# Optimization experiments

Measured on AMD Instinct MI355X. Metric: run time of the kernel, lower is better.

The kernel has to match this reference:

```python
import jax, jax.numpy as jnp
import numpy as np

B, S, D, H = 2, 2048, 1024, 16
DH = D // H  # depth per head = 64


def setup_inputs() -> dict:
    key = jax.random.key(0)
    ks = jax.random.split(key, 5)
    sc = 0.02
    return {
        "x": jax.random.normal(ks[0], (B, S, D), dtype=jnp.float32),
        "Wq": jax.random.normal(ks[1], (D, D), dtype=jnp.float32) * sc,
        "bq": jnp.zeros((D,), dtype=jnp.float32),
        "Wk": jax.random.normal(ks[2], (D, D), dtype=jnp.float32) * sc,
        "bk": jnp.zeros((D,), dtype=jnp.float32),
        "Wv": jax.random.normal(ks[3], (D, D), dtype=jnp.float32) * sc,
        "bv": jnp.zeros((D,), dtype=jnp.float32),
        "Wo": jax.random.normal(ks[4], (D, D), dtype=jnp.float32) * sc,
        "bo": jnp.zeros((D,), dtype=jnp.float32),
    }


def _split_heads(t):
    # [B,S,D] -> [B,H,S,DH]
    return t.reshape(B, S, H, DH).transpose(0, 2, 1, 3)


def reference(x, Wq, bq, Wk, bk, Wv, bv, Wo, bo):
    q = _split_heads(x @ Wq + bq)
    k = _split_heads(x @ Wk + bk)
    v = _split_heads(x @ Wv + bv)
    scale = 1.0 / jnp.sqrt(jnp.float32(DH))
    logits = jnp.einsum("bhqd,bhkd->bhqk", q, k) * scale  # [B,H,S,S]
    attn = jax.nn.softmax(logits, axis=-1)
    ctx = jnp.einsum("bhqk,bhkd->bhqd", attn, v)
    ctx = ctx.transpose(0, 2, 1, 3).reshape(B, S, D)
    # dropout is identity at inference
    return ctx @ Wo + bo
```

## Files before the change

### kernel.cpp

```cpp
#include <hip/hip_runtime.h>
#include <hip/hip_bf16.h>

#define S_LEN   2048
#define D_MODEL 1024
#define NHEAD   16
#define DHEAD   64
#define M_ROWS  4096
#define BHEADS  32
#define MEG     1048576

typedef __attribute__((ext_vector_type(8)))  short short8;
typedef __attribute__((ext_vector_type(4)))  float f32x4;
typedef __attribute__((ext_vector_type(16))) float f32x16;
typedef __attribute__((ext_vector_type(4)))  unsigned short us4;
typedef __attribute__((ext_vector_type(2)))  unsigned int uint2v;
typedef __attribute__((ext_vector_type(4)))  unsigned int uint4v;

extern "C" __device__ float __ocml_native_exp2_f32(float);

__device__ __forceinline__ unsigned short f2b(float f) {
    unsigned int u = __builtin_bit_cast(unsigned int, f);
    return (unsigned short)((u + 0x7FFFu + ((u >> 16) & 1u)) >> 16);
}

__device__ __forceinline__ unsigned int cvtpk(float lo, float hi) {
    unsigned int r;
    asm("v_cvt_pk_bf16_f32 %0, %1, %2" : "=v"(r) : "v"(lo), "v"(hi));
    return r;
}

__device__ __forceinline__ float b2f(unsigned short b) {
    return __builtin_bit_cast(float, (unsigned int)b << 16);
}

#define GLOAD16(gp, lp) __builtin_amdgcn_global_load_lds(                     \
        (const __attribute__((address_space(1))) void*)(gp),                  \
        (__attribute__((address_space(3))) void*)(lp), 16, 0, 0)

#define STAGE_OFS(lane) ((((lane) & 3) ^ (((lane) >> 3) & 3)) * 8)

#define ZERO16(v) do { _Pragma("unroll")                                      \
    for (int z_ = 0; z_ < 16; ++z_) (v)[z_] = 0.f; } while (0)

__global__ __launch_bounds__(256) void prep(
    const float* __restrict__ x, unsigned short* __restrict__ xb,
    const float* __restrict__ Wq, const float* __restrict__ Wk,
    const float* __restrict__ Wv, const float* __restrict__ Wo,
    unsigned short* __restrict__ Wqt, unsigned short* __restrict__ Wkt,
    unsigned short* __restrict__ Wvt, unsigned short* __restrict__ Wot)
{
    const int z = blockIdx.z;
    const int tx = threadIdx.x, ty = threadIdx.y;
    if (z == 4) {
        const int blk = blockIdx.y * 32 + blockIdx.x;
        const int base = (blk * 256 + ty * 32 + tx) * 4;
        #pragma unroll
        for (int r = 0; r < 4; ++r) {
            const int i = base + r * (M_ROWS * D_MODEL / 4);
            const float4 v = *(const float4*)&x[i];
            us4 o;
            o.x = f2b(v.x); o.y = f2b(v.y); o.z = f2b(v.z); o.w = f2b(v.w);
            *(us4*)&xb[i] = o;
        }
        return;
    }
    __shared__ float tile[32][33];
    const float* W = z == 0 ? Wq : (z == 1 ? Wk : (z == 2 ? Wv : Wo));
    unsigned short* Wt = z == 0 ? Wqt : (z == 1 ? Wkt : (z == 2 ? Wvt : Wot));
    const int n0 = blockIdx.x * 32, k0 = blockIdx.y * 32;
    #pragma unroll
    for (int i = 0; i < 4; ++i)
        tile[ty + i * 8][tx] = W[(size_t)(k0 + ty + i * 8) * D_MODEL + n0 + tx];
    __syncthreads();
    #pragma unroll
    for (int i = 0; i < 4; ++i)
        Wt[(size_t)(n0 + ty + i * 8) * D_MODEL + k0 + tx] = f2b(tile[tx][ty + i * 8]);
}

__global__ __launch_bounds__(256) void gemm_qkv(
    const unsigned short* __restrict__ xb,
    const unsigned short* __restrict__ Wqt, const unsigned short* __restrict__ Wkt,
    const unsigned short* __restrict__ Wvt,
    const float* __restrict__ bq, const float* __restrict__ bk,
    const float* __restrict__ bv,
    unsigned short* __restrict__ Qb, unsigned short* __restrict__ Kb,
    unsigned short* __restrict__ Vt)
{
    __shared__ unsigned short As[2][128][32];
    __shared__ unsigned short Bs[2][128][32];

    const int z = blockIdx.z;
    const unsigned short* Wt = z == 0 ? Wqt : (z == 1 ? Wkt : Wvt);
    const float* bias = z == 0 ? bq : (z == 1 ? bk : bv);

    const int t = threadIdx.x, lane = t & 63, w = t >> 6;
    const int wm = w >> 1, wn = w & 1;
    const int bm = blockIdx.y * 128, bn = blockIdx.x * 128;
    const int lr = lane >> 2, lc = STAGE_OFS(lane);
    const int lm = lane & 15, quad = lane >> 4;
    const int qo = (quad ^ ((lm >> 1) & 3)) * 8;

    f32x4 acc[4][4] = {};

    #pragma unroll
    for (int i = 0; i < 2; ++i) {
        const int c = 2 * w + i;
        GLOAD16(xb + (size_t)(bm + c * 16 + lr) * D_MODEL + lc, &As[0][c * 16][0]);
        GLOAD16(Wt + (size_t)(bn + c * 16 + lr) * D_MODEL + lc, &Bs[0][c * 16][0]);
    }
    __syncthreads();

    for (int it = 0; it < 32; ++it) {
        const int cur = it & 1;
        if (it + 1 < 32) {
            const int kt = (it + 1) * 32;
            #pragma unroll
            for (int i = 0; i < 2; ++i) {
                const int c = 2 * w + i;
                GLOAD16(xb + (size_t)(bm + c * 16 + lr) * D_MODEL + kt + lc,
                        &As[cur ^ 1][c * 16][0]);
                GLOAD16(Wt + (size_t)(bn + c * 16 + lr) * D_MODEL + kt + lc,
                        &Bs[cur ^ 1][c * 16][0]);
            }
        }

        short8 af[4], bfr[4];
        #pragma unroll
        for (int mi = 0; mi < 4; ++mi)
            af[mi] = *(const short8*)&As[cur][wm * 64 + mi * 16 + lm][qo];
        #pragma unroll
        for (int ni = 0; ni < 4; ++ni)
            bfr[ni] = *(const short8*)&Bs[cur][wn * 64 + ni * 16 + lm][qo];
        #pragma unroll
        for (int mi = 0; mi < 4; ++mi)
            #pragma unroll
            for (int ni = 0; ni < 4; ++ni)
                acc[mi][ni] = __builtin_amdgcn_mfma_f32_16x16x32_bf16(
                    af[mi], bfr[ni], acc[mi][ni], 0, 0, 0);

        __syncthreads();
    }

    float bb[4];
    #pragma unroll
    for (int ni = 0; ni < 4; ++ni)
        bb[ni] = bias[bn + wn * 64 + ni * 16 + lm];
    const float scale = (z == 0) ? 0.18033688011112042f : 1.0f;

    if (z < 2) {
        unsigned short* Out = (z == 0) ? Qb : Kb;
        #pragma unroll
        for (int mi = 0; mi < 4; ++mi)
            #pragma unroll
            for (int r = 0; r < 4; ++r) {
                const int row = bm + wm * 64 + mi * 16 + quad * 4 + r;
                const int b = row >> 11, s = row & 2047;
                #pragma unroll
                for (int ni = 0; ni < 4; ++ni) {
                    const int col = bn + wn * 64 + ni * 16 + lm;
                    const int h = col >> 6, d = col & 63;
                    Out[(((size_t)(b * NHEAD + h)) * S_LEN + s) * DHEAD + d] =
                        f2b((acc[mi][ni][r] + bb[ni]) * scale);
                }
            }
    } else {
        #pragma unroll
        for (int mi = 0; mi < 4; ++mi) {
            const int row0 = bm + wm * 64 + mi * 16 + quad * 4;
            const int b = row0 >> 11, s0 = row0 & 2047;
            #pragma unroll
            for (int ni = 0; ni < 4; ++ni) {
                const int col = bn + wn * 64 + ni * 16 + lm;
                const int h = col >> 6, d = col & 63;
                us4 pk;
                pk.x = f2b(acc[mi][ni][0] + bb[ni]);
                pk.y = f2b(acc[mi][ni][1] + bb[ni]);
                pk.z = f2b(acc[mi][ni][2] + bb[ni]);
                pk.w = f2b(acc[mi][ni][3] + bb[ni]);
                *(us4*)&Vt[(((size_t)(b * NHEAD + h)) * DHEAD + d) * S_LEN + s0] = pk;
            }
        }
    }
}

__global__ __launch_bounds__(256) void gemm_out(
    const unsigned short* __restrict__ Ab, const unsigned short* __restrict__ Wot,
    const float* __restrict__ bo, float* __restrict__ out)
{
    __shared__ unsigned short As[2][64][32];
    __shared__ unsigned short Bs[2][128][32];

    const int t = threadIdx.x, lane = t & 63, w = t >> 6;
    const int wm = w & 1, wn = w >> 1;
    const int bm = blockIdx.y * 64, bn = blockIdx.x * 128;
    const int lr = lane >> 2, lc = STAGE_OFS(lane);
    const int lm = lane & 15, quad = lane >> 4;
    const int qo = (quad ^ ((lm >> 1) & 3)) * 8;

    f32x4 acc[2][4] = {};

    GLOAD16(Ab + (size_t)(bm + w * 16 + lr) * D_MODEL + lc, &As[0][w * 16][0]);
    #pragma unroll
    for (int i = 0; i < 2; ++i)
        GLOAD16(Wot + (size_t)(bn + w * 32 + i * 16 + lr) * D_MODEL + lc,
                &Bs[0][w * 32 + i * 16][0]);
    __syncthreads();

    for (int it = 0; it < 32; ++it) {
        const int cur = it & 1;
        if (it + 1 < 32) {
            const int kt = (it + 1) * 32;
            GLOAD16(Ab + (size_t)(bm + w * 16 + lr) * D_MODEL + kt + lc,
                    &As[cur ^ 1][w * 16][0]);
            #pragma unroll
            for (int i = 0; i < 2; ++i)
                GLOAD16(Wot + (size_t)(bn + w * 32 + i * 16 + lr) * D_MODEL + kt + lc,
                        &Bs[cur ^ 1][w * 32 + i * 16][0]);
        }

        short8 af[2], bfr[4];
        #pragma unroll
        for (int mi = 0; mi < 2; ++mi)
            af[mi] = *(const short8*)&As[cur][wm * 32 + mi * 16 + lm][qo];
        #pragma unroll
        for (int ni = 0; ni < 4; ++ni)
            bfr[ni] = *(const short8*)&Bs[cur][wn * 64 + ni * 16 + lm][qo];
        #pragma unroll
        for (int mi = 0; mi < 2; ++mi)
            #pragma unroll
            for (int ni = 0; ni < 4; ++ni)
                acc[mi][ni] = __builtin_amdgcn_mfma_f32_16x16x32_bf16(
                    af[mi], bfr[ni], acc[mi][ni], 0, 0, 0);

        __syncthreads();
    }

    float bb[4];
    #pragma unroll
    for (int ni = 0; ni < 4; ++ni)
        bb[ni] = bo[bn + wn * 64 + ni * 16 + lm];

    #pragma unroll
    for (int mi = 0; mi < 2; ++mi)
        #pragma unroll
        for (int r = 0; r < 4; ++r) {
            const int row = bm + wm * 32 + mi * 16 + quad * 4 + r;
            #pragma unroll
            for (int ni = 0; ni < 4; ++ni) {
                const int col = bn + wn * 64 + ni * 16 + lm;
                out[(size_t)row * D_MODEL + col] = acc[mi][ni][r] + bb[ni];
            }
        }
}

__global__ __launch_bounds__(256, 2) void attn_mfma(
    const unsigned short* __restrict__ Q, const unsigned short* __restrict__ K,
    const unsigned short* __restrict__ V, unsigned short* __restrict__ Cx)
{
    __shared__ __align__(16) unsigned char raw[65536];
    unsigned short (*Qs)[128][32] = (unsigned short (*)[128][32])raw;

    const int t = threadIdx.x, lane = t & 63, w = t >> 6;
    const int q5 = lane & 31, hi = lane >> 5;
    const int lr = lane >> 2, lcs = STAGE_OFS(lane);
    const int id  = blockIdx.y * 16 + blockIdx.x;
    const int swz = (id & 7) * 64 + (id >> 3);
    const int q0 = (swz & 15) * 128, bh = swz >> 4;
    const int sw = (q5 >> 1) & 3;
    int sbo[4];
    #pragma unroll
    for (int sb = 0; sb < 4; ++sb) sbo[sb] = (sb ^ sw) * 8;

    const unsigned short* Qh = Q + (size_t)bh * (S_LEN * DHEAD);
    const unsigned short* Kh = K + (size_t)bh * (S_LEN * DHEAD);
    const unsigned short* Vh = V + (size_t)bh * (DHEAD * S_LEN);

    #pragma unroll
    for (int i = 0; i < 2; ++i)
        #pragma unroll
        for (int c = 0; c < 2; ++c)
            GLOAD16(Qh + (size_t)(q0 + w * 32 + c * 16 + lr) * DHEAD + i * 32 + lcs,
                    &Qs[i][w * 32 + c * 16][0]);
    __syncthreads();

    short8 qf[4];
    #pragma unroll
    for (int c = 0; c < 4; ++c)
        qf[c] = *(const short8*)&Qs[c >> 1][w * 32 + q5][sbo[(c & 1) * 2 + hi]];
    __syncthreads();

    short8 onesf;
    #pragma unroll
    for (int j = 0; j < 8; ++j) onesf[j] = (short)0x3F80;

    #define STAGE_KV(IT, BUF) do {                                            \
        const int kt_ = (IT) * 128;                                           \
        unsigned short* ksb_ = (unsigned short*)(raw + (BUF) * 32768);        \
        unsigned short* vsb_ = ksb_ + 8192;                                   \
        _Pragma("unroll")                                                     \
        for (int c_ = 0; c_ < 2; ++c_)                                        \
            _Pragma("unroll")                                                 \
            for (int i_ = 0; i_ < 2; ++i_)                                    \
                GLOAD16(Kh + (size_t)(kt_ + c_ * 64 + w * 16 + lr) * DHEAD    \
                            + i_ * 32 + lcs,                                  \
                        ksb_ + (i_ * 128 + c_ * 64 + w * 16) * 32);           \
        _Pragma("unroll")                                                     \
        for (int i_ = 0; i_ < 4; ++i_)                                        \
            GLOAD16(Vh + (size_t)(w * 16 + lr) * S_LEN + kt_ + i_ * 32 + lcs, \
                    vsb_ + (i_ * 64 + w * 16) * 32);                          \
    } while (0)

    f32x16 acc[2];
    f32x16 acc_l;
    ZERO16(acc[0]); ZERO16(acc[1]); ZERO16(acc_l);

    STAGE_KV(0, 0);

    for (int it = 0; it < 16; ++it) {
        const int cur = it & 1;
        __syncthreads();
        if (it + 1 < 16)
            STAGE_KV(it + 1, cur ^ 1);

        const unsigned short* ks = (const unsigned short*)(raw + cur * 32768);
        const unsigned short* vs = ks + 8192;

        #pragma unroll
        for (int mt = 0; mt < 4; ++mt) {
            f32x16 sf;
            ZERO16(sf);
            __builtin_amdgcn_s_setprio(1);
            #pragma unroll
            for (int c = 0; c < 4; ++c) {
                const short8 kf = *(const short8*)
                    &ks[((c >> 1) * 128 + mt * 32 + q5) * 32
                        + sbo[(c & 1) * 2 + hi]];
                sf = __builtin_amdgcn_mfma_f32_32x32x16_bf16(kf, qf[c], sf, 0, 0, 0);
            }
            __builtin_amdgcn_s_setprio(0);

            #pragma unroll
            for (int pp = 0; pp < 2; ++pp) {
                float p[8];
                #pragma unroll
                for (int e = 0; e < 8; ++e)
                    p[e] = __ocml_native_exp2_f32(sf[pp * 8 + e]);
                const unsigned int dA = cvtpk(p[0], p[1]);
                const unsigned int dB = cvtpk(p[2], p[3]);
                const unsigned int sA = cvtpk(p[4], p[5]);
                const unsigned int sB = cvtpk(p[6], p[7]);
                const uint2v wA = __builtin_amdgcn_permlane32_swap(dA, sA, false, false);
                const uint2v wB = __builtin_amdgcn_permlane32_swap(dB, sB, false, false);
                uint4v wrds;
                wrds.x = wA.x; wrds.y = wB.x; wrds.z = wA.y; wrds.w = wB.y;
                const short8 pf = __builtin_bit_cast(short8, wrds);
                __builtin_amdgcn_s_setprio(1);
                acc_l = __builtin_amdgcn_mfma_f32_32x32x16_bf16(
                    pf, onesf, acc_l, 0, 0, 0);
                #pragma unroll
                for (int nt = 0; nt < 2; ++nt) {
                    const short8 vf = *(const short8*)
                        &vs[(mt * 64 + nt * 32 + q5) * 32 + sbo[pp * 2 + hi]];
                    acc[nt] = __builtin_amdgcn_mfma_f32_32x32x16_bf16(
                        pf, vf, acc[nt], 0, 0, 0);
                }
                __builtin_amdgcn_s_setprio(0);
            }
        }
    }
    #undef STAGE_KV

    const int b = bh >> 4, h = bh & 15;
    #pragma unroll
    for (int reg = 0; reg < 16; ++reg) {
        const int row = (reg & 3) + 8 * (reg >> 2) + 4 * hi;
        const float inv = 1.f / acc_l[reg];
        const int q = q0 + w * 32 + row;
        unsigned short* dst = &Cx[((size_t)(b * S_LEN + q)) * D_MODEL + h * 64];
        dst[q5]      = f2b(acc[0][reg] * inv);
        dst[32 + q5] = f2b(acc[1][reg] * inv);
    }
}

extern "C" void kernel_launch(void* const* d_in, const int* in_sizes, int n_in,
                              void* d_out, int out_size, void* d_ws, size_t ws_size,
                              hipStream_t stream)
{
    const float* x  = (const float*)d_in[0];
    const float* Wq = (const float*)d_in[1];
    const float* bq = (const float*)d_in[2];
    const float* Wk = (const float*)d_in[3];
    const float* bk = (const float*)d_in[4];
    const float* Wv = (const float*)d_in[5];
    const float* bv = (const float*)d_in[6];
    const float* Wo = (const float*)d_in[7];
    const float* bo = (const float*)d_in[8];
    float* out = (float*)d_out;

    unsigned short* base = (unsigned short*)d_ws;
    unsigned short* Wot   = base;
    unsigned short* Qb    = base + 1 * MEG;
    unsigned short* Kb    = base + 5 * MEG;
    unsigned short* Vt    = base + 9 * MEG;
    unsigned short* xb    = base + 13 * MEG;
    unsigned short* Wqt   = base + 17 * MEG;
    unsigned short* Wkt   = base + 18 * MEG;
    unsigned short* Wvt   = base + 19 * MEG;
    unsigned short* Cxb   = xb;

    prep<<<dim3(32, 32, 5), dim3(32, 8), 0, stream>>>(
        x, xb, Wq, Wk, Wv, Wo, Wqt, Wkt, Wvt, Wot);

    gemm_qkv<<<dim3(D_MODEL / 128, M_ROWS / 128, 3), dim3(256), 0, stream>>>(
        xb, Wqt, Wkt, Wvt, bq, bk, bv, Qb, Kb, Vt);

    attn_mfma<<<dim3(S_LEN / 128, BHEADS), dim3(256), 0, stream>>>(
        Qb, Kb, Vt, Cxb);

    gemm_out<<<dim3(D_MODEL / 128, M_ROWS / 64), dim3(256), 0, stream>>>(
        Cxb, Wot, bo, out);
}
```

Measured before the change: 195.3 us.

## Load attention K/V fragments directly from global memory and swizzle GEMM tile order

The attention kernel no longer stages Q, K and V through double-buffered shared memory with block-wide barriers. Each wave now loads its MFMA fragments straight from global memory into registers, software-pipelined one 64-key tile ahead. The QKV and output GEMMs also remap block indices with a swizzle so that neighbouring blocks share tiles in cache. This removes LDS traffic and __syncthreads, but every wave in a block re-reads the same K/V from global/L2 and register pressure rises, which could hurt occupancy or expose latency.

Result: slower. 264.8 us (+35.6%).

```diff
diff --git a/kernel.cpp b/kernel.cpp
--- a/kernel.cpp
+++ b/kernel.cpp
@@ -27,10 +27,6 @@
     unsigned int r;
     asm("v_cvt_pk_bf16_f32 %0, %1, %2" : "=v"(r) : "v"(lo), "v"(hi));
     return r;
-}
-
-__device__ __forceinline__ float b2f(unsigned short b) {
-    return __builtin_bit_cast(float, (unsigned int)b << 16);
 }
 
 #define GLOAD16(gp, lp) __builtin_amdgcn_global_load_lds(                     \
@@ -89,13 +85,18 @@
     __shared__ unsigned short As[2][128][32];
     __shared__ unsigned short Bs[2][128][32];
 
-    const int z = blockIdx.z;
+    const int id  = (blockIdx.z * 32 + blockIdx.y) * 8 + blockIdx.x;
+    const int swz = (id & 7) * 96 + (id >> 3);
+    const int z   = swz >> 8;
+    const int rem = swz & 255;
+    const int bm  = (rem >> 3) * 128;
+    const int bn  = (rem & 7) * 128;
+
     const unsigned short* Wt = z == 0 ? Wqt : (z == 1 ? Wkt : Wvt);
     const float* bias = z == 0 ? bq : (z == 1 ? bk : bv);
 
     const int t = threadIdx.x, lane = t & 63, w = t >> 6;
     const int wm = w >> 1, wn = w & 1;
-    const int bm = blockIdx.y * 128, bn = blockIdx.x * 128;
     const int lr = lane >> 2, lc = STAGE_OFS(lane);
     const int lm = lane & 15, quad = lane >> 4;
     const int qo = (quad ^ ((lm >> 1) & 3)) * 8;
@@ -190,9 +191,13 @@
     __shared__ unsigned short As[2][64][32];
     __shared__ unsigned short Bs[2][128][32];
 
+    const int id  = blockIdx.y * 8 + blockIdx.x;
+    const int swz = (id & 7) * 64 + (id >> 3);
+    const int bm  = (swz >> 3) * 64;
+    const int bn  = (swz & 7) * 128;
+
     const int t = threadIdx.x, lane = t & 63, w = t >> 6;
     const int wm = w & 1, wn = w >> 1;
-    const int bm = blockIdx.y * 64, bn = blockIdx.x * 128;
     const int lr = lane >> 2, lc = STAGE_OFS(lane);
     const int lm = lane & 15, quad = lane >> 4;
     const int qo = (quad ^ ((lm >> 1) & 3)) * 8;
@@ -257,118 +262,95 @@
     const unsigned short* __restrict__ Q, const unsigned short* __restrict__ K,
     const unsigned short* __restrict__ V, unsigned short* __restrict__ Cx)
 {
-    __shared__ __align__(16) unsigned char raw[65536];
-    unsigned short (*Qs)[128][32] = (unsigned short (*)[128][32])raw;
-
     const int t = threadIdx.x, lane = t & 63, w = t >> 6;
     const int q5 = lane & 31, hi = lane >> 5;
-    const int lr = lane >> 2, lcs = STAGE_OFS(lane);
     const int id  = blockIdx.y * 16 + blockIdx.x;
     const int swz = (id & 7) * 64 + (id >> 3);
     const int q0 = (swz & 15) * 128, bh = swz >> 4;
-    const int sw = (q5 >> 1) & 3;
-    int sbo[4];
-    #pragma unroll
-    for (int sb = 0; sb < 4; ++sb) sbo[sb] = (sb ^ sw) * 8;
 
     const unsigned short* Qh = Q + (size_t)bh * (S_LEN * DHEAD);
     const unsigned short* Kh = K + (size_t)bh * (S_LEN * DHEAD);
     const unsigned short* Vh = V + (size_t)bh * (DHEAD * S_LEN);
 
-    #pragma unroll
-    for (int i = 0; i < 2; ++i)
-        #pragma unroll
-        for (int c = 0; c < 2; ++c)
-            GLOAD16(Qh + (size_t)(q0 + w * 32 + c * 16 + lr) * DHEAD + i * 32 + lcs,
-                    &Qs[i][w * 32 + c * 16][0]);
-    __syncthreads();
+    int fo[4];
+    #pragma unroll
+    for (int c = 0; c < 4; ++c)
+        fo[c] = (c >> 1) * 32 + ((c & 1) * 2 + hi) * 8;
 
     short8 qf[4];
     #pragma unroll
     for (int c = 0; c < 4; ++c)
-        qf[c] = *(const short8*)&Qs[c >> 1][w * 32 + q5][sbo[(c & 1) * 2 + hi]];
-    __syncthreads();
+        qf[c] = *(const short8*)&Qh[(size_t)(q0 + w * 32 + q5) * DHEAD + fo[c]];
 
     short8 onesf;
     #pragma unroll
     for (int j = 0; j < 8; ++j) onesf[j] = (short)0x3F80;
 
-    #define STAGE_KV(IT, BUF) do {                                            \
-        const int kt_ = (IT) * 128;                                           \
-        unsigned short* ksb_ = (unsigned short*)(raw + (BUF) * 32768);        \
-        unsigned short* vsb_ = ksb_ + 8192;                                   \
-        _Pragma("unroll")                                                     \
-        for (int c_ = 0; c_ < 2; ++c_)                                        \
-            _Pragma("unroll")                                                 \
-            for (int i_ = 0; i_ < 2; ++i_)                                    \
-                GLOAD16(Kh + (size_t)(kt_ + c_ * 64 + w * 16 + lr) * DHEAD    \
-                            + i_ * 32 + lcs,                                  \
-                        ksb_ + (i_ * 128 + c_ * 64 + w * 16) * 32);           \
-        _Pragma("unroll")                                                     \
-        for (int i_ = 0; i_ < 4; ++i_)                                        \
-            GLOAD16(Vh + (size_t)(w * 16 + lr) * S_LEN + kt_ + i_ * 32 + lcs, \
-                    vsb_ + (i_ * 64 + w * 16) * 32);                          \
-    } while (0)
+    short8 kf[4][2];
+    short8 vf[4][2];
+
+    #define LOAD_KF(KT) do { _Pragma("unroll")                                \
+        for (int c_ = 0; c_ < 4; ++c_) { _Pragma("unroll")                    \
+            for (int mt_ = 0; mt_ < 2; ++mt_)                                 \
+                kf[c_][mt_] = *(const short8*)                                \
+                    &Kh[(size_t)((KT) + mt_ * 32 + q5) * DHEAD + fo[c_]];     \
+        } } while (0)
+    #define LOAD_VF(KT) do { _Pragma("unroll")                                \
+        for (int c_ = 0; c_ < 4; ++c_) { _Pragma("unroll")                    \
+            for (int nt_ = 0; nt_ < 2; ++nt_)                                 \
+                vf[c_][nt_] = *(const short8*)                                \
+                    &Vh[(size_t)(nt_ * 32 + q5) * S_LEN + (KT) + fo[c_]];     \
+        } } while (0)
 
     f32x16 acc[2];
     f32x16 acc_l;
     ZERO16(acc[0]); ZERO16(acc[1]); ZERO16(acc_l);
 
-    STAGE_KV(0, 0);
-
-    for (int it = 0; it < 16; ++it) {
-        const int cur = it & 1;
-        __syncthreads();
-        if (it + 1 < 16)
-            STAGE_KV(it + 1, cur ^ 1);
-
-        const unsigned short* ks = (const unsigned short*)(raw + cur * 32768);
-        const unsigned short* vs = ks + 8192;
-
-        #pragma unroll
-        for (int mt = 0; mt < 4; ++mt) {
-            f32x16 sf;
-            ZERO16(sf);
-            __builtin_amdgcn_s_setprio(1);
-            #pragma unroll
-            for (int c = 0; c < 4; ++c) {
-                const short8 kf = *(const short8*)
-                    &ks[((c >> 1) * 128 + mt * 32 + q5) * 32
-                        + sbo[(c & 1) * 2 + hi]];
-                sf = __builtin_amdgcn_mfma_f32_32x32x16_bf16(kf, qf[c], sf, 0, 0, 0);
-            }
-            __builtin_amdgcn_s_setprio(0);
-
-            #pragma unroll
-            for (int pp = 0; pp < 2; ++pp) {
-                float p[8];
-                #pragma unroll
-                for (int e = 0; e < 8; ++e)
-                    p[e] = __ocml_native_exp2_f32(sf[pp * 8 + e]);
-                const unsigned int dA = cvtpk(p[0], p[1]);
-                const unsigned int dB = cvtpk(p[2], p[3]);
-                const unsigned int sA = cvtpk(p[4], p[5]);
-                const unsigned int sB = cvtpk(p[6], p[7]);
-                const uint2v wA = __builtin_amdgcn_permlane32_swap(dA, sA, false, false);
-                const uint2v wB = __builtin_amdgcn_permlane32_swap(dB, sB, false, false);
-                uint4v wrds;
-                wrds.x = wA.x; wrds.y = wB.x; wrds.z = wA.y; wrds.w = wB.y;
-                const short8 pf = __builtin_bit_cast(short8, wrds);
-                __builtin_amdgcn_s_setprio(1);
-                acc_l = __builtin_amdgcn_mfma_f32_32x32x16_bf16(
-                    pf, onesf, acc_l, 0, 0, 0);
-                #pragma unroll
-                for (int nt = 0; nt < 2; ++nt) {
-                    const short8 vf = *(const short8*)
-                        &vs[(mt * 64 + nt * 32 + q5) * 32 + sbo[pp * 2 + hi]];
-                    acc[nt] = __builtin_amdgcn_mfma_f32_32x32x16_bf16(
-                        pf, vf, acc[nt], 0, 0, 0);
-                }
-                __builtin_amdgcn_s_setprio(0);
-            }
-        }
-    }
-    #undef STAGE_KV
+    LOAD_KF(0);
+    LOAD_VF(0);
+
+    for (int it = 0; it < 32; ++it) {
+        const int kt = it * 64;
+
+        f32x16 sf[2];
+        ZERO16(sf[0]); ZERO16(sf[1]);
+        #pragma unroll
+        for (int c = 0; c < 4; ++c)
+            #pragma unroll
+            for (int mt = 0; mt < 2; ++mt)
+                sf[mt] = __builtin_amdgcn_mfma_f32_32x32x16_bf16(
+                    kf[c][mt], qf[c], sf[mt], 0, 0, 0);
+
+        if (it + 1 < 32) LOAD_KF(kt + 64);
+
+        #pragma unroll
+        for (int c = 0; c < 4; ++c) {
+            const int mt = c >> 1, pp = c & 1;
+            float p[8];
+            #pragma unroll
+            for (int e = 0; e < 8; ++e)
+                p[e] = __ocml_native_exp2_f32(sf[mt][pp * 8 + e]);
+            const unsigned int dA = cvtpk(p[0], p[1]);
+            const unsigned int dB = cvtpk(p[2], p[3]);
+            const unsigned int sA = cvtpk(p[4], p[5]);
+            const unsigned int sB = cvtpk(p[6], p[7]);
+            const uint2v wA = __builtin_amdgcn_permlane32_swap(dA, sA, false, false);
+            const uint2v wB = __builtin_amdgcn_permlane32_swap(dB, sB, false, false);
+            uint4v wrds;
+            wrds.x = wA.x; wrds.y = wB.x; wrds.z = wA.y; wrds.w = wB.y;
+            const short8 pf = __builtin_bit_cast(short8, wrds);
+            acc_l = __builtin_amdgcn_mfma_f32_32x32x16_bf16(
+                pf, onesf, acc_l, 0, 0, 0);
+            #pragma unroll
+            for (int nt = 0; nt < 2; ++nt)
+                acc[nt] = __builtin_amdgcn_mfma_f32_32x32x16_bf16(
+                    pf, vf[c][nt], acc[nt], 0, 0, 0);
+        }
+
+        if (it + 1 < 32) LOAD_VF(kt + 64);
+    }
+    #undef LOAD_KF
+    #undef LOAD_VF
 
     const int b = bh >> 4, h = bh & 15;
     #pragma unroll
```
